# Optimization experiments

Measured on AMD Instinct MI355X. Metric: run time of the kernel, lower is better.

The kernel has to match this reference:

```python
import jax, jax.numpy as jnp
import numpy as np

NUM_CLASSES = 91
COST_CLASS, COST_BBOX, COST_GIOU = 1.0, 5.0, 2.0
W_CE, W_BBOX, W_GIOU = 2.0, 2.5, 2.0
EOS_COEF = 0.1
B, Q, T = 64, 300, 25


def box_cxcywh_to_xyxy(x):
    cx, cy, w, h = x[..., 0], x[..., 1], x[..., 2], x[..., 3]
    return jnp.stack([cx - 0.5 * w, cy - 0.5 * h, cx + 0.5 * w, cy + 0.5 * h], axis=-1)


def giou_pairwise(b1, b2):
    # b1 [N,4], b2 [M,4] in xyxy -> [N,M]
    area1 = (b1[:, 2] - b1[:, 0]) * (b1[:, 3] - b1[:, 1])
    area2 = (b2[:, 2] - b2[:, 0]) * (b2[:, 3] - b2[:, 1])
    lt = jnp.maximum(b1[:, None, :2], b2[None, :, :2])
    rb = jnp.minimum(b1[:, None, 2:], b2[None, :, 2:])
    wh = jnp.clip(rb - lt, 0.0)
    inter = wh[..., 0] * wh[..., 1]
    union = area1[:, None] + area2[None, :] - inter
    iou = inter / union
    lti = jnp.minimum(b1[:, None, :2], b2[None, :, :2])
    rbi = jnp.maximum(b1[:, None, 2:], b2[None, :, 2:])
    whi = jnp.clip(rbi - lti, 0.0)
    areai = whi[..., 0] * whi[..., 1]
    return iou - (areai - union) / areai


def giou_elementwise(b1, b2):
    # b1,b2 [N,4] xyxy -> [N]
    area1 = (b1[:, 2] - b1[:, 0]) * (b1[:, 3] - b1[:, 1])
    area2 = (b2[:, 2] - b2[:, 0]) * (b2[:, 3] - b2[:, 1])
    lt = jnp.maximum(b1[:, :2], b2[:, :2])
    rb = jnp.minimum(b1[:, 2:], b2[:, 2:])
    wh = jnp.clip(rb - lt, 0.0)
    inter = wh[:, 0] * wh[:, 1]
    union = area1 + area2 - inter
    iou = inter / union
    lti = jnp.minimum(b1[:, :2], b2[:, :2])
    rbi = jnp.maximum(b1[:, 2:], b2[:, 2:])
    whi = jnp.clip(rbi - lti, 0.0)
    areai = whi[:, 0] * whi[:, 1]
    return iou - (areai - union) / areai


def _lsa(cost):
    # Jonker-Volgenant shortest augmenting path; same optimum as scipy linear_sum_assignment
    cost = np.asarray(cost, dtype=np.float64)
    transposed = cost.shape[0] > cost.shape[1]
    if transposed:
        cost = cost.T
    n, m = cost.shape  # n <= m
    u = np.zeros(n + 1)
    v = np.zeros(m + 1)
    p = np.zeros(m + 1, dtype=np.int64)
    way = np.zeros(m + 1, dtype=np.int64)
    for i in range(1, n + 1):
        p[0] = i
        j0 = 0
        minv = np.full(m + 1, np.inf)
        used = np.zeros(m + 1, dtype=bool)
        while True:
            used[j0] = True
            i0 = p[j0]
            cur = cost[i0 - 1, :] - u[i0] - v[1:]
            free = ~used[1:]
            better = free & (cur < minv[1:])
            minv[1:][better] = cur[better]
            way[1:][better] = j0
            masked = np.where(free, minv[1:], np.inf)
            j1 = int(np.argmin(masked)) + 1
            delta = minv[j1]
            u[p[used]] += delta
            v[used] -= delta
            minv[~used] -= delta
            j0 = j1
            if p[j0] == 0:
                break
        while j0:
            j1 = way[j0]
            p[j0] = p[j1]
            j0 = j1
    rows, cols = [], []
    for j in range(1, m + 1):
        if p[j] != 0:
            rows.append(p[j] - 1)
            cols.append(j - 1)
    rows = np.asarray(rows, dtype=np.int64)
    cols = np.asarray(cols, dtype=np.int64)
    if transposed:
        rows, cols = cols, rows
    order = np.argsort(rows)
    return rows[order], cols[order]


def _match(pred_logits, pred_boxes, tgt_labels, tgt_boxes):
    # builds the full cross-batch cost matrix exactly like the torch module, then
    # solves per-image rectangular assignment on the host (non-differentiable)
    log_prob = jax.nn.log_softmax(pred_logits.reshape(B * Q, NUM_CLASSES + 1), axis=-1)
    out_bbox = pred_boxes.reshape(B * Q, 4)
    tgt_ids = tgt_labels.reshape(B * T)
    tgt_bb = tgt_boxes.reshape(B * T, 4)
    cost_class = -log_prob[:, tgt_ids]                                        # [BQ, BT]
    cost_bbox = jnp.abs(out_bbox[:, None, :] - tgt_bb[None, :, :]).sum(-1)    # L1 cdist
    cost_giou = -giou_pairwise(box_cxcywh_to_xyxy(out_bbox), box_cxcywh_to_xyxy(tgt_bb))
    C = COST_BBOX * cost_bbox + COST_CLASS * cost_class + COST_GIOU * cost_giou
    Cn = np.asarray(jax.lax.stop_gradient(C.reshape(B, Q, B * T)))
    src = np.zeros((B, T), dtype=np.int64)
    tgt = np.zeros((B, T), dtype=np.int64)
    for b in range(B):
        r, c = _lsa(Cn[b, :, b * T:(b + 1) * T])
        src[b] = r
        tgt[b] = c
    batch_idx = jnp.repeat(jnp.arange(B), T)
    return batch_idx, jnp.asarray(src.reshape(-1)), jnp.asarray(tgt.reshape(-1))


def _losses(pred_logits, pred_boxes, tgt_labels, tgt_boxes, batch_idx, src_idx, tgt_idx):
    num_t = batch_idx.shape[0]
    matched_labels = tgt_labels[batch_idx, tgt_idx]
    target_classes = jnp.full((B, Q), NUM_CLASSES, dtype=jnp.int32)
    target_classes = target_classes.at[batch_idx, src_idx].set(matched_labels)
    empty_weight = jnp.ones(NUM_CLASSES + 1, dtype=pred_logits.dtype).at[-1].set(EOS_COEF)
    logp = jax.nn.log_softmax(pred_logits, axis=-1)
    nll = -jnp.take_along_axis(logp, target_classes[..., None], axis=-1)[..., 0]
    w = empty_weight[target_classes]
    loss_ce = (w * nll).sum() / w.sum()
    src_b = pred_boxes[batch_idx, src_idx]
    tgt_b = tgt_boxes[batch_idx, tgt_idx]
    loss_bbox = jnp.abs(src_b - tgt_b).sum() / num_t
    loss_giou = (1.0 - giou_elementwise(box_cxcywh_to_xyxy(src_b), box_cxcywh_to_xyxy(tgt_b))).sum() / num_t
    l_ce = W_CE * loss_ce
    l_bb = W_BBOX * loss_bbox
    l_gi = W_GIOU * loss_giou
    return jnp.stack([l_ce, l_bb, l_gi, l_ce + l_bb + l_gi])


def setup_inputs() -> dict:
    key = jax.random.key(0)
    k1, k2, k3, k4 = jax.random.split(key, 4)
    pred_logits = jax.random.normal(k1, (B, Q, NUM_CLASSES + 1), dtype=jnp.float32)
    pred_boxes = jax.random.uniform(k2, (B, Q, 4), dtype=jnp.float32, minval=0.05, maxval=0.95)
    tgt_labels = jax.random.randint(k3, (B, T), 0, NUM_CLASSES)
    tgt_boxes = jax.random.uniform(k4, (B, T, 4), dtype=jnp.float32, minval=0.05, maxval=0.95)
    return {"pred_logits": pred_logits, "pred_boxes": pred_boxes, "tgt_labels": tgt_labels, "tgt_boxes": tgt_boxes}


def reference(pred_logits, pred_boxes, tgt_labels, tgt_boxes):
    batch_idx, src_idx, tgt_idx = _match(pred_logits, pred_boxes, tgt_labels, tgt_boxes)
    # returns [loss_ce, loss_bbox, loss_giou, loss_total] (already weight-scaled)
    return _losses(pred_logits, pred_boxes, tgt_labels, tgt_boxes, batch_idx, src_idx, tgt_idx)
```

## Files before the change

kernel.cpp:

```cpp
#include <hip/hip_runtime.h>
#include <math.h>

constexpr int B_ = 64;
constexpr int Q_ = 300;
constexpr int T_ = 25;
constexpr int NCLS = 91;
constexpr int L_ = NCLS + 1;
constexpr float C_BB = 5.0f, C_GI = 2.0f;
constexpr float W_CE = 2.0f, W_BBOX = 2.5f, W_GIOU = 2.0f;
constexpr float EOS = 0.1f;
constexpr int K_ = 5;
constexpr int TPB = 256;

__device__ __forceinline__ unsigned long long ord64(double v) {
    long long bb = __double_as_longlong(v);
    return (bb < 0) ? ~(unsigned long long)bb
                    : ((unsigned long long)bb | 0x8000000000000000ULL);
}
__device__ __forceinline__ double unord64(unsigned long long u) {
    long long bb = (u & 0x8000000000000000ULL) ? (long long)(u & 0x7FFFFFFFFFFFFFFFULL)
                                               : (long long)~u;
    return __longlong_as_double(bb);
}
__device__ __forceinline__ unsigned int ord32(float f) {
    unsigned int b = __float_as_uint(f);
    return (b & 0x80000000u) ? ~b : (b | 0x80000000u);
}

__device__ __forceinline__ float giou_f(const float px[4], float parea,
                                        const float tx[4], float tarea) {
    float ltx = fmaxf(px[0], tx[0]), lty = fmaxf(px[1], tx[1]);
    float rbx = fminf(px[2], tx[2]), rby = fminf(px[3], tx[3]);
    float iw = fmaxf(rbx - ltx, 0.f), ih = fmaxf(rby - lty, 0.f);
    float inter = iw * ih;
    float uni = parea + tarea - inter;
    float iou = inter / uni;
    float lix = fminf(px[0], tx[0]), liy = fminf(px[1], tx[1]);
    float rix = fmaxf(px[2], tx[2]), riy = fmaxf(px[3], tx[3]);
    float aw = fmaxf(rix - lix, 0.f), ah = fmaxf(riy - liy, 0.f);
    float ai = aw * ah;
    return iou - (ai - uni) / ai;
}

__global__ __launch_bounds__(TPB) void fused_kernel(
        const float* __restrict__ logits,
        const float* __restrict__ pboxes,
        const int*   __restrict__ tlabels,
        const float* __restrict__ tboxes,
        double* __restrict__ partial) {
    const int b = blockIdx.x;
    const int tid = threadIdx.x;

    __shared__ float  costL[T_][Q_];
    __shared__ float  lseL[Q_];
    __shared__ int    pL[Q_ + 1];
    __shared__ int    wayL[Q_ + 1];
    __shared__ double uL[T_ + 1];
    __shared__ int    argcolL[T_];
    __shared__ int    mqL[T_];
    __shared__ int    lblL[T_];
    __shared__ int    lblq[Q_];
    __shared__ float  tbL[T_][4];
    __shared__ float  txL[T_][4];
    __shared__ float  taL[T_];
    __shared__ double wsum[4][3];

    if (tid < T_) {
        lblL[tid] = tlabels[b * T_ + tid];
        mqL[tid] = 0;
        float c0 = tboxes[(size_t)(b * T_ + tid) * 4 + 0];
        float c1 = tboxes[(size_t)(b * T_ + tid) * 4 + 1];
        float c2 = tboxes[(size_t)(b * T_ + tid) * 4 + 2];
        float c3 = tboxes[(size_t)(b * T_ + tid) * 4 + 3];
        tbL[tid][0] = c0; tbL[tid][1] = c1; tbL[tid][2] = c2; tbL[tid][3] = c3;
        float x0 = c0 - 0.5f * c2, y0 = c1 - 0.5f * c3;
        float x1 = c0 + 0.5f * c2, y1 = c1 + 0.5f * c3;
        txL[tid][0] = x0; txL[tid][1] = y0; txL[tid][2] = x1; txL[tid][3] = y1;
        taL[tid] = (x1 - x0) * (y1 - y0);
    }
    for (int j = tid; j <= Q_; j += TPB) { pL[j] = 0; wayL[j] = 0; }
    for (int q = tid; q < Q_; q += TPB) lblq[q] = NCLS;
    __syncthreads();

    const float* lgb = logits + (size_t)b * Q_ * L_;
    const float* pbb = pboxes + (size_t)b * Q_ * 4;

    for (int q = tid; q < Q_; q += TPB) {
        const float4* lr4 = (const float4*)(lgb + (size_t)q * L_);
        float m0 = -INFINITY, m1 = -INFINITY, m2 = -INFINITY, m3 = -INFINITY;
        for (int c = 0; c < 23; ++c) {
            float4 v = lr4[c];
            m0 = fmaxf(m0, v.x); m1 = fmaxf(m1, v.y);
            m2 = fmaxf(m2, v.z); m3 = fmaxf(m3, v.w);
        }
        float mx = fmaxf(fmaxf(m0, m1), fmaxf(m2, m3));
        float s0 = 0.f, s1 = 0.f, s2 = 0.f, s3 = 0.f;
        for (int c = 0; c < 23; ++c) {
            float4 v = lr4[c];
            s0 += expf(v.x - mx); s1 += expf(v.y - mx);
            s2 += expf(v.z - mx); s3 += expf(v.w - mx);
        }
        float lz = mx + logf((s0 + s1) + (s2 + s3));
        lseL[q] = lz;

        float p0 = pbb[(size_t)q * 4 + 0], p1 = pbb[(size_t)q * 4 + 1];
        float p2 = pbb[(size_t)q * 4 + 2], p3 = pbb[(size_t)q * 4 + 3];
        float px[4] = { p0 - 0.5f * p2, p1 - 0.5f * p3, p0 + 0.5f * p2, p1 + 0.5f * p3 };
        float parea = (px[2] - px[0]) * (px[3] - px[1]);

#pragma unroll
        for (int t = 0; t < T_; ++t) {
            float cls = lz - lgb[(size_t)q * L_ + lblL[t]];
            float l1 = fabsf(p0 - tbL[t][0]) + fabsf(p1 - tbL[t][1]) +
                       fabsf(p2 - tbL[t][2]) + fabsf(p3 - tbL[t][3]);
            float tx[4] = { txL[t][0], txL[t][1], txL[t][2], txL[t][3] };
            float g = giou_f(px, parea, tx, taL[t]);
            costL[t][q] = C_BB * l1 + cls - C_GI * g;
        }
    }
    __syncthreads();

    {
        int w = tid >> 6, lane = tid & 63;
        for (int t = w; t < T_; t += 4) {
            unsigned long long best = ~0ULL;
#pragma unroll
            for (int k = 0; k < K_; ++k) {
                int col = lane + 64 * k;
                if (col < Q_) {
                    unsigned long long kk =
                        ((unsigned long long)ord32(costL[t][col]) << 32) | (unsigned)col;
                    if (kk < best) best = kk;
                }
            }
#pragma unroll
            for (int off = 1; off < 64; off <<= 1) {
                unsigned long long o = __shfl_xor(best, off);
                if (o < best) best = o;
            }
            if (lane == 0) {
                int jc = (int)(best & 0xFFFFFFFFULL);
                argcolL[t] = jc;
                uL[t + 1] = (double)costL[t][jc];
            }
        }
    }
    __syncthreads();

    if (tid < 64) {
        int win = tid;
        if (tid < T_) {
            int myc = argcolL[tid];
            for (int j = 0; j < T_; ++j) {
                int oc = argcolL[j];
                if (oc == myc && j < win) win = j;
            }
            if (win == tid) pL[myc + 1] = tid + 1;
        }
        unsigned long long mb = __ballot(tid < T_ && win == tid);
        unsigned int freemask = (~(unsigned int)mb) & ((1u << T_) - 1);

        double v0[K_], minv[K_], stampv[K_];
        int pReg[K_];
        bool usedk[K_], validk[K_];
#pragma unroll
        for (int k = 0; k < K_; ++k) {
            int col = tid + 64 * k;
            validk[k] = col < Q_;
            v0[k] = 0.0;
            stampv[k] = 0.0; usedk[k] = false; minv[k] = INFINITY;
            pReg[k] = validk[k] ? pL[col + 1] : 0;
        }

        for (int iter = 0; iter < 64 && freemask; ++iter) {
            int t = __builtin_ctz(freemask);
            freemask &= freemask - 1;

            double am1 = INFINITY, am2 = INFINITY;
            int aj1 = Q_;
            const float* crow = &costL[t][0];
#pragma unroll
            for (int k = 0; k < K_; ++k) {
                if (validk[k]) {
                    int col = tid + 64 * k;
                    double h = (double)crow[col] - v0[k];
                    if (h < am1) { am2 = am1; am1 = h; aj1 = col; }
                    else if (h < am2) { am2 = h; }
                }
            }
#pragma unroll
            for (int off = 1; off < 64; off <<= 1) {
                double om1 = __shfl_xor(am1, off);
                double om2 = __shfl_xor(am2, off);
                int    oj1 = __shfl_xor(aj1, off);
                if (om1 < am1 || (om1 == am1 && oj1 < aj1)) {
                    am2 = fmin(am1, om2); am1 = om1; aj1 = oj1;
                } else {
                    am2 = fmin(am2, om1);
                }
            }
            int j1 = aj1;
            int owner = j1 & 63, k1 = j1 >> 6;
            int prev = pL[j1 + 1];
            bool lowered = (am1 < am2);
            if (tid == owner && lowered) {
#pragma unroll
                for (int k = 0; k < K_; ++k)
                    if (k == k1) v0[k] -= (am2 - am1);
            }
            if (tid == owner) {
#pragma unroll
                for (int k = 0; k < K_; ++k)
                    if (k == k1) pReg[k] = t + 1;
            }
            if (tid == 0) { pL[j1 + 1] = t + 1; uL[t + 1] = am2; }
            if (prev) freemask |= 1u << (prev - 1);
        }

        for (int i = 1; i <= T_; ++i) {
            if (!((freemask >> (i - 1)) & 1u)) continue;
            if (tid == 0) pL[0] = i;
#pragma unroll
            for (int k = 0; k < K_; ++k) { minv[k] = INFINITY; usedk[k] = false; }
            double S = 0.0;
            int j0 = 0, i0 = i;
            double u0i0 = uL[i];

            for (int step = 0; step < 512; ++step) {
                double a = u0i0 - S;
                const float* crow = &costL[i0 - 1][0];
                unsigned long long bk = ~0ULL;
                unsigned int ba = 0xFFFFFFFFu;
#pragma unroll
                for (int k = 0; k < K_; ++k) {
                    if (validk[k] && !usedk[k]) {
                        int col = tid + 64 * k;
                        double cur = (double)crow[col] - a - v0[k];
                        if (cur < minv[k]) { minv[k] = cur; wayL[col + 1] = j0; }
                        unsigned long long kk = ord64(minv[k]);
                        unsigned int aux = ((unsigned)(col + 1) << 5) | (unsigned)pReg[k];
                        if (kk < bk || (kk == bk && aux < ba)) { bk = kk; ba = aux; }
                    }
                }
#pragma unroll
                for (int off = 1; off < 64; off <<= 1) {
                    unsigned long long ok = __shfl_xor(bk, off);
                    unsigned int oa = __shfl_xor(ba, off);
                    if (ok < bk || (ok == bk && oa < ba)) { bk = ok; ba = oa; }
                }
                int j1  = (int)(ba >> 5);
                int i0n = (int)(ba & 31u);
                double Snew = unord64(bk);
                S = Snew;
                j0 = j1;
                if (i0n == 0) break;
                int owner = (j1 - 1) & 63, k1 = (j1 - 1) >> 6;
                if (tid == owner) {
#pragma unroll
                    for (int k = 0; k < K_; ++k)
                        if (k == k1) { usedk[k] = true; stampv[k] = Snew; }
                }
                i0 = i0n;
                u0i0 = uL[i0];
            }

#pragma unroll
            for (int k = 0; k < K_; ++k) {
                if (validk[k] && usedk[k]) {
                    double d = S - stampv[k];
                    v0[k] -= d;
                    uL[pReg[k]] += d;
                }
            }
            if (tid == 0) {
                uL[i] += S;
                int jj = j0;
                while (jj) { int jn = wayL[jj]; pL[jj] = pL[jn]; jj = jn; }
            }
#pragma unroll
            for (int k = 0; k < K_; ++k)
                if (validk[k]) pReg[k] = pL[tid + 1 + 64 * k];
        }

#pragma unroll
        for (int k = 0; k < K_; ++k)
            if (validk[k] && pReg[k] > 0) mqL[pReg[k] - 1] = tid + 64 * k;
        if (tid < T_) lblq[mqL[tid]] = lblL[tid];
    }
    __syncthreads();

    double ce = 0.0, sb = 0.0, sg = 0.0;
    for (int q = tid; q < Q_; q += TPB) {
        int label = lblq[q];
        float nll = lseL[q] - lgb[(size_t)q * L_ + label];
        float w = (label == NCLS) ? EOS : 1.0f;
        ce += (double)(w * nll);
    }
    if (tid < T_) {
        int q = mqL[tid];
        float p0 = pbb[(size_t)q * 4 + 0], p1 = pbb[(size_t)q * 4 + 1];
        float p2 = pbb[(size_t)q * 4 + 2], p3 = pbb[(size_t)q * 4 + 3];
        sb = (double)(fabsf(p0 - tbL[tid][0]) + fabsf(p1 - tbL[tid][1]) +
                      fabsf(p2 - tbL[tid][2]) + fabsf(p3 - tbL[tid][3]));
        float px[4] = { p0 - 0.5f * p2, p1 - 0.5f * p3, p0 + 0.5f * p2, p1 + 0.5f * p3 };
        float parea = (px[2] - px[0]) * (px[3] - px[1]);
        float tx[4] = { txL[tid][0], txL[tid][1], txL[tid][2], txL[tid][3] };
        float g = giou_f(px, parea, tx, taL[tid]);
        sg = (double)(1.0f - g);
    }
#pragma unroll
    for (int off = 1; off < 64; off <<= 1) {
        ce += __shfl_xor(ce, off);
        sb += __shfl_xor(sb, off);
        sg += __shfl_xor(sg, off);
    }
    if ((tid & 63) == 0) {
        int w = tid >> 6;
        wsum[w][0] = ce; wsum[w][1] = sb; wsum[w][2] = sg;
    }
    __syncthreads();
    if (tid == 0) {
        double a0 = 0, a1 = 0, a2 = 0;
        for (int w = 0; w < 4; ++w) { a0 += wsum[w][0]; a1 += wsum[w][1]; a2 += wsum[w][2]; }
        partial[(size_t)b * 3 + 0] = a0;
        partial[(size_t)b * 3 + 1] = a1;
        partial[(size_t)b * 3 + 2] = a2;
    }
}

__global__ __launch_bounds__(64) void finalize_kernel(const double* __restrict__ partial,
                                                      float* __restrict__ out) {
    int tid = threadIdx.x;
    double a = partial[(size_t)tid * 3 + 0];
    double c = partial[(size_t)tid * 3 + 1];
    double g = partial[(size_t)tid * 3 + 2];
#pragma unroll
    for (int off = 1; off < 64; off <<= 1) {
        a += __shfl_xor(a, off);
        c += __shfl_xor(c, off);
        g += __shfl_xor(g, off);
    }
    if (tid == 0) {
        float lce = W_CE * (float)(a / 3360.0);
        float lbb = W_BBOX * (float)(c / 1600.0);
        float lgi = W_GIOU * (float)(g / 1600.0);
        out[0] = lce;
        out[1] = lbb;
        out[2] = lgi;
        out[3] = lce + lbb + lgi;
    }
}

extern "C" void kernel_launch(void* const* d_in, const int* in_sizes, int n_in,
                              void* d_out, int out_size, void* d_ws, size_t ws_size,
                              hipStream_t stream) {
    (void)in_sizes; (void)n_in; (void)out_size; (void)ws_size;
    const float* logits  = (const float*)d_in[0];
    const float* pboxes  = (const float*)d_in[1];
    const int*   tlabels = (const int*)d_in[2];
    const float* tboxes  = (const float*)d_in[3];
    float* out = (float*)d_out;
    double* partial = (double*)d_ws;

    fused_kernel<<<B_, TPB, 0, stream>>>(logits, pboxes, tlabels, tboxes, partial);
    finalize_kernel<<<1, 64, 0, stream>>>(partial, out);
}
```

Measured before the change: 42.43 us.

## Pack keys into single 64-bit words and use DPP/swizzle wave reductions in LSA

The auction and Dijkstra wave-level reductions now pack the value plus its index and row tag into one 64-bit key by truncating low mantissa bits, and reduce it with DPP row ops and ds_swizzle instead of six shfl_xor rounds. The dual variables u move from shared memory into per-lane registers read with __shfl, and pL is written back once after the auction phase. This is meant to cut the per-step latency of the serial augmenting-path loop. Truncating the mantissa bits can change tie-breaking or pick a slightly different minimum, which risks a different optimal assignment in near-tie cases. The auction iteration cap also drops from 64 to 48.

```diff
diff --git a/kernel.cpp b/kernel.cpp
--- a/kernel.cpp
+++ b/kernel.cpp
@@ -25,6 +25,50 @@
 __device__ __forceinline__ unsigned int ord32(float f) {
     unsigned int b = __float_as_uint(f);
     return (b & 0x80000000u) ? ~b : (b | 0x80000000u);
+}
+__device__ __forceinline__ unsigned long long pack14(double v, unsigned aux) {
+    return (ord64(v) & ~16383ULL) | (unsigned long long)aux;
+}
+__device__ __forceinline__ unsigned long long pack9(double v, unsigned col) {
+    return (ord64(v) & ~511ULL) | (unsigned long long)col;
+}
+
+template <int CTRL>
+__device__ __forceinline__ unsigned long long dppb(unsigned long long b) {
+    int lo = __builtin_amdgcn_update_dpp(0, (int)(unsigned)b, CTRL, 0xF, 0xF, true);
+    int hi = __builtin_amdgcn_update_dpp(0, (int)(unsigned)(b >> 32), CTRL, 0xF, 0xF, true);
+    return ((unsigned long long)(unsigned)hi << 32) | (unsigned)lo;
+}
+__device__ __forceinline__ unsigned long long swz16(unsigned long long b) {
+    int lo = __builtin_amdgcn_ds_swizzle((int)(unsigned)b, 0x401F);
+    int hi = __builtin_amdgcn_ds_swizzle((int)(unsigned)(b >> 32), 0x401F);
+    return ((unsigned long long)(unsigned)hi << 32) | (unsigned)lo;
+}
+
+__device__ __forceinline__ unsigned long long wavemin(unsigned long long b) {
+    { unsigned long long o = __shfl_xor(b, 32); if (o < b) b = o; }
+    { unsigned long long o = swz16(b);      if (o < b) b = o; }
+    { unsigned long long o = dppb<0x140>(b); if (o < b) b = o; }
+    { unsigned long long o = dppb<0x141>(b); if (o < b) b = o; }
+    { unsigned long long o = dppb<0x4E>(b);  if (o < b) b = o; }
+    { unsigned long long o = dppb<0xB1>(b);  if (o < b) b = o; }
+    return b;
+}
+__device__ __forceinline__ void red2(unsigned long long& k1, unsigned long long& k2,
+                                     unsigned long long o1, unsigned long long o2) {
+    unsigned long long n1 = o1 < k1 ? o1 : k1;
+    unsigned long long ls = o1 < k1 ? k1 : o1;
+    unsigned long long n2 = k2 < o2 ? k2 : o2;
+    n2 = ls < n2 ? ls : n2;
+    k1 = n1; k2 = n2;
+}
+__device__ __forceinline__ void wavemin2(unsigned long long& k1, unsigned long long& k2) {
+    red2(k1, k2, __shfl_xor(k1, 32), __shfl_xor(k2, 32));
+    red2(k1, k2, swz16(k1), swz16(k2));
+    red2(k1, k2, dppb<0x140>(k1), dppb<0x140>(k2));
+    red2(k1, k2, dppb<0x141>(k1), dppb<0x141>(k2));
+    red2(k1, k2, dppb<0x4E>(k1),  dppb<0x4E>(k2));
+    red2(k1, k2, dppb<0xB1>(k1),  dppb<0xB1>(k2));
 }
 
 __device__ __forceinline__ float giou_f(const float px[4], float parea,
@@ -56,6 +100,7 @@
     __shared__ int    pL[Q_ + 1];
     __shared__ int    wayL[Q_ + 1];
     __shared__ double uL[T_ + 1];
+    __shared__ double uStage[32];
     __shared__ int    argcolL[T_];
     __shared__ int    mqL[T_];
     __shared__ int    lblL[T_];
@@ -133,11 +178,7 @@
                     if (kk < best) best = kk;
                 }
             }
-#pragma unroll
-            for (int off = 1; off < 64; off <<= 1) {
-                unsigned long long o = __shfl_xor(best, off);
-                if (o < best) best = o;
-            }
+            best = wavemin(best);
             if (lane == 0) {
                 int jc = (int)(best & 0xFFFFFFFFULL);
                 argcolL[t] = jc;
@@ -163,6 +204,7 @@
         double v0[K_], minv[K_], stampv[K_];
         int pReg[K_];
         bool usedk[K_], validk[K_];
+        double ureg = (tid >= 1 && tid <= T_) ? uL[tid] : 0.0;
 #pragma unroll
         for (int k = 0; k < K_; ++k) {
             int col = tid + 64 * k;
@@ -172,50 +214,42 @@
             pReg[k] = validk[k] ? pL[col + 1] : 0;
         }
 
-        for (int iter = 0; iter < 64 && freemask; ++iter) {
+        for (int iter = 0; iter < 48 && freemask; ++iter) {
             int t = __builtin_ctz(freemask);
             freemask &= freemask - 1;
-
-            double am1 = INFINITY, am2 = INFINITY;
-            int aj1 = Q_;
             const float* crow = &costL[t][0];
+            unsigned long long k1 = ~0ULL, k2 = ~0ULL;
 #pragma unroll
             for (int k = 0; k < K_; ++k) {
                 if (validk[k]) {
                     int col = tid + 64 * k;
-                    double h = (double)crow[col] - v0[k];
-                    if (h < am1) { am2 = am1; am1 = h; aj1 = col; }
-                    else if (h < am2) { am2 = h; }
-                }
-            }
-#pragma unroll
-            for (int off = 1; off < 64; off <<= 1) {
-                double om1 = __shfl_xor(am1, off);
-                double om2 = __shfl_xor(am2, off);
-                int    oj1 = __shfl_xor(aj1, off);
-                if (om1 < am1 || (om1 == am1 && oj1 < aj1)) {
-                    am2 = fmin(am1, om2); am1 = om1; aj1 = oj1;
-                } else {
-                    am2 = fmin(am2, om1);
-                }
-            }
-            int j1 = aj1;
-            int owner = j1 & 63, k1 = j1 >> 6;
-            int prev = pL[j1 + 1];
-            bool lowered = (am1 < am2);
-            if (tid == owner && lowered) {
+                    unsigned long long kk = pack9((double)crow[col] - v0[k], (unsigned)col);
+                    if (kk < k1) { k2 = k1; k1 = kk; }
+                    else if (kk < k2) { k2 = kk; }
+                }
+            }
+            wavemin2(k1, k2);
+            int j1 = (int)(k1 & 511ULL);
+            double am1 = unord64(k1 & ~511ULL);
+            double am2 = unord64(k2 & ~511ULL);
+            int owner = j1 & 63, k1i = j1 >> 6;
+            int psel = pReg[0];
+#pragma unroll
+            for (int k = 1; k < K_; ++k)
+                if (k1i == k) psel = pReg[k];
+            int prev = __shfl(psel, owner);
+            if (tid == owner) {
 #pragma unroll
                 for (int k = 0; k < K_; ++k)
-                    if (k == k1) v0[k] -= (am2 - am1);
-            }
-            if (tid == owner) {
-#pragma unroll
-                for (int k = 0; k < K_; ++k)
-                    if (k == k1) pReg[k] = t + 1;
-            }
-            if (tid == 0) { pL[j1 + 1] = t + 1; uL[t + 1] = am2; }
+                    if (k == k1i) { v0[k] -= (am2 - am1); pReg[k] = t + 1; }
+            }
+            if (tid == t + 1) ureg = am2;
             if (prev) freemask |= 1u << (prev - 1);
         }
+
+#pragma unroll
+        for (int k = 0; k < K_; ++k)
+            if (validk[k]) pL[tid + 1 + 64 * k] = pReg[k];
 
         for (int i = 1; i <= T_; ++i) {
             if (!((freemask >> (i - 1)) & 1u)) continue;
@@ -224,56 +258,52 @@
             for (int k = 0; k < K_; ++k) { minv[k] = INFINITY; usedk[k] = false; }
             double S = 0.0;
             int j0 = 0, i0 = i;
-            double u0i0 = uL[i];
+            double u0i0 = __shfl(ureg, i);
 
             for (int step = 0; step < 512; ++step) {
                 double a = u0i0 - S;
                 const float* crow = &costL[i0 - 1][0];
                 unsigned long long bk = ~0ULL;
-                unsigned int ba = 0xFFFFFFFFu;
 #pragma unroll
                 for (int k = 0; k < K_; ++k) {
                     if (validk[k] && !usedk[k]) {
                         int col = tid + 64 * k;
                         double cur = (double)crow[col] - a - v0[k];
                         if (cur < minv[k]) { minv[k] = cur; wayL[col + 1] = j0; }
-                        unsigned long long kk = ord64(minv[k]);
-                        unsigned int aux = ((unsigned)(col + 1) << 5) | (unsigned)pReg[k];
-                        if (kk < bk || (kk == bk && aux < ba)) { bk = kk; ba = aux; }
+                        unsigned long long kk = pack14(
+                            minv[k], ((unsigned)(col + 1) << 5) | (unsigned)pReg[k]);
+                        if (kk < bk) bk = kk;
                     }
                 }
-#pragma unroll
-                for (int off = 1; off < 64; off <<= 1) {
-                    unsigned long long ok = __shfl_xor(bk, off);
-                    unsigned int oa = __shfl_xor(ba, off);
-                    if (ok < bk || (ok == bk && oa < ba)) { bk = ok; ba = oa; }
-                }
-                int j1  = (int)(ba >> 5);
-                int i0n = (int)(ba & 31u);
-                double Snew = unord64(bk);
+                bk = wavemin(bk);
+                int j1  = (int)((bk >> 5) & 511ULL);
+                int i0n = (int)(bk & 31ULL);
+                double Snew = unord64(bk & ~16383ULL);
                 S = Snew;
                 j0 = j1;
                 if (i0n == 0) break;
-                int owner = (j1 - 1) & 63, k1 = (j1 - 1) >> 6;
+                int owner = (j1 - 1) & 63, k1i = (j1 - 1) >> 6;
                 if (tid == owner) {
 #pragma unroll
                     for (int k = 0; k < K_; ++k)
-                        if (k == k1) { usedk[k] = true; stampv[k] = Snew; }
+                        if (k == k1i) { usedk[k] = true; stampv[k] = Snew; }
                 }
                 i0 = i0n;
-                u0i0 = uL[i0];
-            }
-
+                u0i0 = __shfl(ureg, i0);
+            }
+
+            if (tid <= T_) uStage[tid] = 0.0;
 #pragma unroll
             for (int k = 0; k < K_; ++k) {
                 if (validk[k] && usedk[k]) {
                     double d = S - stampv[k];
                     v0[k] -= d;
-                    uL[pReg[k]] += d;
-                }
-            }
+                    uStage[pReg[k]] = d;
+                }
+            }
+            if (tid >= 1 && tid <= T_) ureg += uStage[tid];
+            if (tid == i) ureg += S;
             if (tid == 0) {
-                uL[i] += S;
                 int jj = j0;
                 while (jj) { int jn = wayL[jj]; pL[jj] = pL[jn]; jj = jn; }
             }
```

Result: faster. 37.22 us (-12.3%).
